# Performance work log

Measured on AMD Instinct MI355X. Metric: run time of the kernel, lower is better.

Reference implementation:

```python
import jax, jax.numpy as jnp
import numpy as np

B, N, IN_F, OUT_F, H = 4, 2048, 128, 128, 4
D = OUT_F // H  # head_dim = 32
NEG_SLOPE = 0.2


def setup_inputs() -> dict:
    key = jax.random.key(0)
    k1, k2, k3, k4, k5 = jax.random.split(key, 5)
    x = jax.random.normal(k1, (B, N, IN_F), dtype=jnp.float32)
    adj = jax.random.randint(k2, (N, N), 0, 2, dtype=jnp.int32)
    adj = adj.at[jnp.arange(N), jnp.arange(N)].set(1)  # self-loops
    # xavier-uniform-like init
    lim_w = float(np.sqrt(6.0 / (IN_F + OUT_F)))
    W = jax.random.uniform(k3, (OUT_F, IN_F), minval=-lim_w, maxval=lim_w, dtype=jnp.float32)
    lim_a = float(np.sqrt(6.0 / (H + D)))
    a_src = jax.random.uniform(k4, (H, D), minval=-lim_a, maxval=lim_a, dtype=jnp.float32)
    a_dst = jax.random.uniform(k5, (H, D), minval=-lim_a, maxval=lim_a, dtype=jnp.float32)
    return {"x": x, "adj": adj, "W": W, "a_src": a_src, "a_dst": a_dst}


def reference(x, adj, W, a_src, a_dst):
    Bx, Nx, _ = x.shape
    # linear projection: (B,N,out) -> (B,N,H,D)
    h = jnp.einsum('bni,oi->bno', x, W).reshape(Bx, Nx, H, D)
    e_src = jnp.einsum('bnhd,hd->bnh', h, a_src)  # (B,N,H)
    e_dst = jnp.einsum('bnhd,hd->bnh', h, a_dst)  # (B,N,H)
    # scores: (B,N_src,H,N_dst)
    scores = jax.nn.leaky_relu(
        e_src[:, :, :, None] + e_dst.transpose(0, 2, 1)[:, None, :, :],
        negative_slope=NEG_SLOPE,
    )
    mask = adj[None, :, None, :]  # (1,N,1,N)
    scores = jnp.where(mask == 0, -jnp.inf, scores)
    attn = jax.nn.softmax(scores, axis=-1)  # (B,N,H,N); dropout is identity at eval
    out = jnp.einsum('bnhm,bmhd->bnhd', attn, h)  # (B,N,H,D)
    return out.reshape(Bx, Nx, H * D)
```

## Files before the change

kernel.cpp:

```cpp
#include <hip/hip_runtime.h>
#include <math.h>

#define BB 4
#define NN 2048
#define FF 128
#define HH 4
#define DD 32
#define NEG_SLOPE 0.2f
#define LOG2E 1.4426950408889634f

typedef __attribute__((ext_vector_type(8))) short short8;
typedef __attribute__((ext_vector_type(4))) float floatx4;
typedef __attribute__((ext_vector_type(2))) float floatx2;

__device__ __forceinline__ float exp2_fast(float x) {
#if __has_builtin(__builtin_amdgcn_exp2f)
    return __builtin_amdgcn_exp2f(x);
#else
    return exp2f(x);
#endif
}

__device__ __forceinline__ int bit_mask(unsigned int w, int bit) {
#if __has_builtin(__builtin_amdgcn_sbfe)
    return __builtin_amdgcn_sbfe((int)w, bit, 1);
#else
    return ((int)(w << (31 - bit))) >> 31;
#endif
}

__device__ __forceinline__ unsigned short to_bf16(float f) {
    unsigned int ui = __float_as_uint(f);
    ui += 0x7FFFu + ((ui >> 16) & 1u);
    return (unsigned short)(ui >> 16);
}

__device__ __forceinline__ unsigned int pack2_rtne(float lo, float hi) {
    unsigned int ul = __float_as_uint(lo); ul += 0x7FFFu + ((ul >> 16) & 1u);
    unsigned int uh = __float_as_uint(hi); uh += 0x7FFFu + ((uh >> 16) & 1u);
    return (ul >> 16) | (uh & 0xFFFF0000u);
}

__global__ __launch_bounds__(256) void k_prep(const float* __restrict__ x,
                                              const float* __restrict__ W,
                                              const float* __restrict__ a_src,
                                              const float* __restrict__ a_dst,
                                              const int* __restrict__ adj,
                                              unsigned short* __restrict__ ht,
                                              float* __restrict__ es_t,
                                              float* __restrict__ ed_t,
                                              unsigned int* __restrict__ bits) {
    __shared__ unsigned short wbf[128][144];
    __shared__ unsigned short hbf[128][24];
    __shared__ float vs_s[HH][FF], vd_s[HH][FF];
    __shared__ float as_s[FF], ad_s[FF];
    int t = threadIdx.x;

    if (blockIdx.x >= 512) {
        int idx = (blockIdx.x - 512) * 256 + t;
        int n = idx >> 6, w = idx & 63;
        const int4* base = (const int4*)(adj + (size_t)n * NN + w * 32);
        unsigned int word = 0;
#pragma unroll
        for (int q = 0; q < 8; ++q) {
            int4 a = base[q];
            word |= ((unsigned int)(a.x & 1)) << (q * 4 + 0);
            word |= ((unsigned int)(a.y & 1)) << (q * 4 + 1);
            word |= ((unsigned int)(a.z & 1)) << (q * 4 + 2);
            word |= ((unsigned int)(a.w & 1)) << (q * 4 + 3);
        }
        bits[idx] = word;
        return;
    }

    int m0g = blockIdx.x * 16;
    int b = m0g >> 11;
    int m_block = m0g & 2047;

    if (t < FF) { as_s[t] = a_src[t]; ad_s[t] = a_dst[t]; }
#pragma unroll
    for (int k = 0; k < 8; ++k) {
        int idx = t + k * 256;
        int row = idx >> 4, ch = idx & 15;
        const float* wp = W + (size_t)row * FF + ch * 8;
        float4 v0 = *(const float4*)wp;
        float4 v1 = *(const float4*)(wp + 4);
        unsigned int u[4];
        u[0] = pack2_rtne(v0.x, v0.y); u[1] = pack2_rtne(v0.z, v0.w);
        u[2] = pack2_rtne(v1.x, v1.y); u[3] = pack2_rtne(v1.z, v1.w);
        *(int4*)&wbf[row][ch * 8] = *(const int4*)u;
    }
    __syncthreads();

    {
        int i = t & 127;
        float acc4[4] = {0.f, 0.f, 0.f, 0.f};
        if (t < 128) {
            for (int o = 0; o < 128; ++o) {
                float wv = __uint_as_float(((unsigned int)wbf[o][i]) << 16);
                acc4[o >> 5] += wv * as_s[o];
            }
#pragma unroll
            for (int hd = 0; hd < 4; ++hd) vs_s[hd][i] = acc4[hd];
        } else {
            for (int o = 0; o < 128; ++o) {
                float wv = __uint_as_float(((unsigned int)wbf[o][i]) << 16);
                acc4[o >> 5] += wv * ad_s[o];
            }
#pragma unroll
            for (int hd = 0; hd < 4; ++hd) vd_s[hd][i] = acc4[hd];
        }
    }

    int wid = t >> 6, lane = t & 63;
    int r = lane & 15, q = lane >> 4;
    floatx4 acc[2] = {{0.f,0.f,0.f,0.f},{0.f,0.f,0.f,0.f}};
    const float* xrow = x + (size_t)(m0g + r) * FF + q * 8;
#pragma unroll
    for (int kk = 0; kk < 4; ++kk) {
        float4 a0 = *(const float4*)(xrow + kk * 32);
        float4 a1 = *(const float4*)(xrow + kk * 32 + 4);
        union { short8 s8; unsigned int u[4]; } af;
        af.u[0] = pack2_rtne(a0.x, a0.y); af.u[1] = pack2_rtne(a0.z, a0.w);
        af.u[2] = pack2_rtne(a1.x, a1.y); af.u[3] = pack2_rtne(a1.z, a1.w);
#pragma unroll
        for (int c = 0; c < 2; ++c) {
            int o = (wid * 2 + c) * 16 + r;
            short8 bf = *(const short8*)&wbf[o][kk * 32 + q * 8];
            acc[c] = __builtin_amdgcn_mfma_f32_16x16x32_bf16(af.s8, bf, acc[c], 0, 0, 0);
        }
    }
#pragma unroll
    for (int c = 0; c < 2; ++c) {
        int o = (wid * 2 + c) * 16 + r;
        unsigned int u2[2];
        u2[0] = pack2_rtne(acc[c][0], acc[c][1]);
        u2[1] = pack2_rtne(acc[c][2], acc[c][3]);
        *(int2*)&hbf[o][q * 4] = *(const int2*)u2;
    }
    __syncthreads();

    if (t < 128) {
        int hd = t >> 5, d = t & 31;
        unsigned short* op = ht + ((size_t)(b * HH + hd) * DD + d) * NN + m_block;
        *(int4*)op       = *(const int4*)&hbf[t][0];
        *(int4*)(op + 8) = *(const int4*)&hbf[t][8];
    }
    {
        int m = t >> 4, sg = t & 15;
        const float* xp = x + (size_t)(m0g + m) * FF + sg * 8;
        float4 x0 = *(const float4*)xp;
        float4 x1 = *(const float4*)(xp + 4);
#pragma unroll
        for (int hd = 0; hd < 4; ++hd) {
            const float* vsp = &vs_s[hd][sg * 8];
            const float* vdp = &vd_s[hd][sg * 8];
            float es = x0.x * vsp[0] + x0.y * vsp[1] + x0.z * vsp[2] + x0.w * vsp[3]
                     + x1.x * vsp[4] + x1.y * vsp[5] + x1.z * vsp[6] + x1.w * vsp[7];
            float ed = x0.x * vdp[0] + x0.y * vdp[1] + x0.z * vdp[2] + x0.w * vdp[3]
                     + x1.x * vdp[4] + x1.y * vdp[5] + x1.z * vdp[6] + x1.w * vdp[7];
#pragma unroll
            for (int k = 1; k < 16; k <<= 1) {
                es += __shfl_xor(es, k);
                ed += __shfl_xor(ed, k);
            }
            if (sg == 0) {
                size_t eb = (size_t)(b * HH + hd) * NN + m_block + m;
                es_t[eb] = es * LOG2E;
                ed_t[eb] = ed * LOG2E;
            }
        }
    }
}

#define HTS 2056
__global__ __launch_bounds__(1024) void k_attn(
        const unsigned short* __restrict__ ht,
        const unsigned int* __restrict__ bits,
        const float* __restrict__ es_t,
        const float* __restrict__ ed_t,
        float* __restrict__ out) {
    __shared__ unsigned short hb[DD * HTS];
    __shared__ float ep[NN * 2];
    int t = threadIdx.x;
    int n0 = blockIdx.x * 128;
    int bh = blockIdx.y;
    int b = bh >> 2, head = bh & 3;

    int wid = t >> 6, lane = t & 63;
    int q = lane >> 4, r = lane & 15;
    int qo = q * 8;
    int half = wid >> 3, wsub = wid & 7;
    int n_l = wsub * 16 + r;

    {
        float2 v = ((const float2*)(ed_t + (size_t)bh * NN))[t];
        float4 o;
        o.x = exp2_fast(v.x); o.y = exp2_fast(NEG_SLOPE * v.x);
        o.z = exp2_fast(v.y); o.w = exp2_fast(NEG_SLOPE * v.y);
        ((float4*)ep)[t] = o;
    }
    {
        const unsigned short* htp = ht + (size_t)bh * DD * NN;
#pragma unroll
        for (int k = 0; k < 8; ++k) {
            int qq = t + k * 1024;
            int d = qq >> 8, cm = qq & 255;
            int4 v = *(const int4*)(htp + (size_t)d * NN + cm * 8);
            *(int4*)&hb[d * HTS + cm * 8] = v;
        }
    }
    int4 bw[8];
    {
        const int4* bp = (const int4*)(bits + (size_t)(n0 + n_l) * 64 + half * 32);
#pragma unroll
        for (int g = 0; g < 8; ++g) bw[g] = bp[g];
    }
    float esv = es_t[(size_t)bh * NN + n0 + n_l];
    floatx2 es2 = {exp2_fast(esv), exp2_fast(NEG_SLOPE * esv)};
    __syncthreads();

    floatx4 acc0 = {0.f, 0.f, 0.f, 0.f};
    floatx4 acc1 = {0.f, 0.f, 0.f, 0.f};
    floatx4 accd = {0.f, 0.f, 0.f, 0.f};
    union { short8 s8; int i[4]; } ones;
    ones.i[0] = 0x3F803F80; ones.i[1] = 0x3F803F80;
    ones.i[2] = 0x3F803F80; ones.i[3] = 0x3F803F80;

    const float* eph = ep + half * 2048;
    const unsigned short* hrow0 = &hb[r * HTS + half * 1024 + qo];
    const unsigned short* hrow1 = hrow0 + 16 * HTS;

#pragma unroll
    for (int g = 0; g < 8; ++g) {
#pragma unroll
        for (int c = 0; c < 4; ++c) {
            unsigned int word = (unsigned int)((&bw[g].x)[c]);
            int mb = (g * 4 + c) * 32;
            unsigned int wq = word >> qo;
            const float* pbase = eph + (mb + qo) * 2;
            union { short8 s8; int i[4]; } af;
#pragma unroll
            for (int jp = 0; jp < 4; ++jp) {
                float4 d2 = *(const float4*)(pbase + jp * 4);
                floatx2 p0 = es2 * (floatx2){d2.x, d2.y};
                floatx2 p1 = es2 * (floatx2){d2.z, d2.w};
                float w0 = fmaxf(p0.x, p0.y);
                float w1 = fmaxf(p1.x, p1.y);
                int m0 = bit_mask(wq, 2 * jp);
                int m1 = bit_mask(wq, 2 * jp + 1);
                w0 = __uint_as_float(__float_as_uint(w0) & (unsigned int)m0);
                w1 = __uint_as_float(__float_as_uint(w1) & (unsigned int)m1);
                af.i[jp] = __builtin_amdgcn_perm(__float_as_uint(w1),
                                                 __float_as_uint(w0),
                                                 0x07060302u);
            }
            short8 b0 = *(const short8*)(hrow0 + mb);
            short8 b1 = *(const short8*)(hrow1 + mb);
            acc0 = __builtin_amdgcn_mfma_f32_16x16x32_bf16(af.s8, b0, acc0, 0, 0, 0);
            acc1 = __builtin_amdgcn_mfma_f32_16x16x32_bf16(af.s8, b1, acc1, 0, 0, 0);
            accd = __builtin_amdgcn_mfma_f32_16x16x32_bf16(af.s8, ones.s8, accd, 0, 0, 0);
        }
    }

    __syncthreads();
    float* scr = (float*)hb;
    if (wid >= 8) {
        int base = ((wid - 8) * 64 + lane) * 12;
        *(floatx4*)&scr[base + 0] = acc0;
        *(floatx4*)&scr[base + 4] = acc1;
        *(floatx4*)&scr[base + 8] = accd;
    }
    __syncthreads();
    if (wid < 8) {
        int base = (wid * 64 + lane) * 12;
        floatx4 p0 = *(const floatx4*)&scr[base + 0];
        floatx4 p1 = *(const floatx4*)&scr[base + 4];
        floatx4 pd = *(const floatx4*)&scr[base + 8];
#pragma unroll
        for (int k = 0; k < 4; ++k) {
            acc0[k] += p0[k]; acc1[k] += p1[k]; accd[k] += pd[k];
        }
#pragma unroll
        for (int reg = 0; reg < 4; ++reg) {
            int nrow = n0 + wsub * 16 + q * 4 + reg;
            float inv = 1.0f / accd[reg];
            float* op = out + ((size_t)(b * NN + nrow)) * FF + head * DD;
            op[r]      = acc0[reg] * inv;
            op[16 + r] = acc1[reg] * inv;
        }
    }
}

extern "C" void kernel_launch(void* const* d_in, const int* in_sizes, int n_in,
                              void* d_out, int out_size, void* d_ws, size_t ws_size,
                              hipStream_t stream) {
    const float* x     = (const float*)d_in[0];
    const int*   adj   = (const int*)d_in[1];
    const float* W     = (const float*)d_in[2];
    const float* a_src = (const float*)d_in[3];
    const float* a_dst = (const float*)d_in[4];
    float* out = (float*)d_out;

    float* es_t = (float*)d_ws;
    float* ed_t = es_t + (size_t)BB * HH * NN;
    unsigned int* bits = (unsigned int*)(ed_t + (size_t)BB * HH * NN);
    unsigned short* ht = (unsigned short*)(bits + (size_t)NN * (NN / 32));

    hipLaunchKernelGGL(k_prep, dim3(1024), dim3(256), 0, stream,
                       x, W, a_src, a_dst, adj, ht, es_t, ed_t, bits);
    hipLaunchKernelGGL(k_attn, dim3(NN / 128, BB * HH), dim3(1024), 0, stream,
                       ht, bits, es_t, ed_t, out);
}
```

Before: 101.9 us.

## Read value features directly from global memory and halve attention block size

The attention kernel no longer stages the per-head bf16 feature matrix (about 128KB) in shared memory. MFMA B operands are now loaded straight from global memory, and the adjacency bit words are loaded per iteration instead of being held in registers. The block shrinks to 512 threads covering 64 rows, which doubles the grid. LDS use drops to the 16KB exp table, so more blocks can fit per CU and the staging cost disappears, at the price of repeated global/L2 reads of the feature data with less favourable access patterns.

```diff
diff --git a/kernel.cpp b/kernel.cpp
--- a/kernel.cpp
+++ b/kernel.cpp
@@ -27,12 +27,6 @@
 #else
     return ((int)(w << (31 - bit))) >> 31;
 #endif
-}
-
-__device__ __forceinline__ unsigned short to_bf16(float f) {
-    unsigned int ui = __float_as_uint(f);
-    ui += 0x7FFFu + ((ui >> 16) & 1u);
-    return (unsigned short)(ui >> 16);
 }
 
 __device__ __forceinline__ unsigned int pack2_rtne(float lo, float hi) {
@@ -173,48 +167,33 @@
     }
 }
 
-#define HTS 2056
-__global__ __launch_bounds__(1024) void k_attn(
+__global__ __launch_bounds__(512) void k_attn(
         const unsigned short* __restrict__ ht,
         const unsigned int* __restrict__ bits,
         const float* __restrict__ es_t,
         const float* __restrict__ ed_t,
         float* __restrict__ out) {
-    __shared__ unsigned short hb[DD * HTS];
     __shared__ float ep[NN * 2];
     int t = threadIdx.x;
-    int n0 = blockIdx.x * 128;
+    int n0 = blockIdx.x * 64;
     int bh = blockIdx.y;
     int b = bh >> 2, head = bh & 3;
 
     int wid = t >> 6, lane = t & 63;
     int q = lane >> 4, r = lane & 15;
     int qo = q * 8;
-    int half = wid >> 3, wsub = wid & 7;
+    int half = wid >> 2, wsub = wid & 3;
     int n_l = wsub * 16 + r;
 
     {
-        float2 v = ((const float2*)(ed_t + (size_t)bh * NN))[t];
-        float4 o;
-        o.x = exp2_fast(v.x); o.y = exp2_fast(NEG_SLOPE * v.x);
-        o.z = exp2_fast(v.y); o.w = exp2_fast(NEG_SLOPE * v.y);
-        ((float4*)ep)[t] = o;
-    }
-    {
-        const unsigned short* htp = ht + (size_t)bh * DD * NN;
-#pragma unroll
-        for (int k = 0; k < 8; ++k) {
-            int qq = t + k * 1024;
-            int d = qq >> 8, cm = qq & 255;
-            int4 v = *(const int4*)(htp + (size_t)d * NN + cm * 8);
-            *(int4*)&hb[d * HTS + cm * 8] = v;
-        }
-    }
-    int4 bw[8];
-    {
-        const int4* bp = (const int4*)(bits + (size_t)(n0 + n_l) * 64 + half * 32);
-#pragma unroll
-        for (int g = 0; g < 8; ++g) bw[g] = bp[g];
+        float4 v = ((const float4*)(ed_t + (size_t)bh * NN))[t];
+        float4 o01, o23;
+        o01.x = exp2_fast(v.x); o01.y = exp2_fast(NEG_SLOPE * v.x);
+        o01.z = exp2_fast(v.y); o01.w = exp2_fast(NEG_SLOPE * v.y);
+        o23.x = exp2_fast(v.z); o23.y = exp2_fast(NEG_SLOPE * v.z);
+        o23.z = exp2_fast(v.w); o23.w = exp2_fast(NEG_SLOPE * v.w);
+        ((float4*)ep)[2 * t]     = o01;
+        ((float4*)ep)[2 * t + 1] = o23;
     }
     float esv = es_t[(size_t)bh * NN + n0 + n_l];
     floatx2 es2 = {exp2_fast(esv), exp2_fast(NEG_SLOPE * esv)};
@@ -228,14 +207,17 @@
     ones.i[2] = 0x3F803F80; ones.i[3] = 0x3F803F80;
 
     const float* eph = ep + half * 2048;
-    const unsigned short* hrow0 = &hb[r * HTS + half * 1024 + qo];
-    const unsigned short* hrow1 = hrow0 + 16 * HTS;
+    const unsigned short* hrow0 = ht + (size_t)bh * DD * NN
+                                  + (size_t)r * NN + half * 1024 + qo;
+    const unsigned short* hrow1 = hrow0 + 16 * NN;
+    const unsigned int* bp = bits + (size_t)(n0 + n_l) * 64 + half * 32;
 
 #pragma unroll
     for (int g = 0; g < 8; ++g) {
+        int4 bwv = *(const int4*)(bp + g * 4);
 #pragma unroll
         for (int c = 0; c < 4; ++c) {
-            unsigned int word = (unsigned int)((&bw[g].x)[c]);
+            unsigned int word = (unsigned int)((&bwv.x)[c]);
             int mb = (g * 4 + c) * 32;
             unsigned int wq = word >> qo;
             const float* pbase = eph + (mb + qo) * 2;
@@ -264,16 +246,16 @@
     }
 
     __syncthreads();
-    float* scr = (float*)hb;
-    if (wid >= 8) {
-        int base = ((wid - 8) * 64 + lane) * 12;
+    float* scr = ep;
+    if (half == 1) {
+        int base = (wsub * 64 + lane) * 12;
         *(floatx4*)&scr[base + 0] = acc0;
         *(floatx4*)&scr[base + 4] = acc1;
         *(floatx4*)&scr[base + 8] = accd;
     }
     __syncthreads();
-    if (wid < 8) {
-        int base = (wid * 64 + lane) * 12;
+    if (half == 0) {
+        int base = (wsub * 64 + lane) * 12;
         floatx4 p0 = *(const floatx4*)&scr[base + 0];
         floatx4 p1 = *(const floatx4*)&scr[base + 4];
         floatx4 pd = *(const floatx4*)&scr[base + 8];
@@ -309,6 +291,6 @@
 
     hipLaunchKernelGGL(k_prep, dim3(1024), dim3(256), 0, stream,
                        x, W, a_src, a_dst, adj, ht, es_t, ed_t, bits);
-    hipLaunchKernelGGL(k_attn, dim3(NN / 128, BB * HH), dim3(1024), 0, stream,
+    hipLaunchKernelGGL(k_attn, dim3(NN / 64, BB * HH), dim3(512), 0, stream,
                        ht, bits, es_t, ed_t, out);
 }
```

Result: slower. 115.2 us (+13.1%).
